# Optimization experiments

Measured on AMD Instinct MI355X. Metric: run time of the kernel, lower is better.

## Reference

```python
import jax, jax.numpy as jnp
import numpy as np

NEG_SLOPE = 0.2  # PyG GATConv default negative_slope
BN_EPS = 1e-5


def _segment_softmax(logits, seg, num_segments):
    # numerically stable softmax over edges grouped by destination node
    m = jax.ops.segment_max(logits, seg, num_segments=num_segments)
    e = jnp.exp(logits - m[seg])
    s = jax.ops.segment_sum(e, seg, num_segments=num_segments)
    return e / s[seg]


def _gat_conv(x, src, dst, W, a_src, a_dst, bias, heads, d_head, concat):
    N = x.shape[0]
    h = (x @ W).reshape(N, heads, d_head)                      # [N, H, D]
    alpha_src = jnp.einsum('nhd,hd->nh', h, a_src)             # [N, H]
    alpha_dst = jnp.einsum('nhd,hd->nh', h, a_dst)             # [N, H]
    logits = jax.nn.leaky_relu(alpha_src[src] + alpha_dst[dst], NEG_SLOPE)  # [E, H]
    alpha = _segment_softmax(logits, dst, N)                   # [E, H]
    msg = h[src] * alpha[:, :, None]                           # [E, H, D]
    out = jax.ops.segment_sum(msg, dst, num_segments=N)        # [N, H, D]
    out = out.reshape(N, heads * d_head) if concat else out.mean(axis=1)
    return out + bias


def setup_inputs() -> dict:
    key = jax.random.key(0)
    ks = jax.random.split(key, 12)
    N, E = 50000, 800000
    in_dim, hidden, out_dim, heads = 256, 128, 2, 4
    d1 = hidden // heads  # 32
    s = 0.05
    return {
        'x': jax.random.normal(ks[0], (N, in_dim), dtype=jnp.float32),
        'edge_index': jax.random.randint(ks[1], (2, E), 0, N, dtype=jnp.int64),
        'W1': jax.random.normal(ks[2], (in_dim, heads * d1), dtype=jnp.float32) * s,
        'att_src1': jax.random.normal(ks[3], (heads, d1), dtype=jnp.float32) * s,
        'att_dst1': jax.random.normal(ks[4], (heads, d1), dtype=jnp.float32) * s,
        'b1': jnp.zeros((heads * d1,), dtype=jnp.float32),
        'bn_gamma': jnp.ones((hidden,), dtype=jnp.float32),
        'bn_beta': jnp.zeros((hidden,), dtype=jnp.float32),
        'bn_mean': jnp.zeros((hidden,), dtype=jnp.float32),
        'bn_var': jnp.ones((hidden,), dtype=jnp.float32),
        'W2': jax.random.normal(ks[5], (hidden, out_dim), dtype=jnp.float32) * s,
        'att_src2': jax.random.normal(ks[6], (1, out_dim), dtype=jnp.float32) * s,
        'att_dst2': jax.random.normal(ks[7], (1, out_dim), dtype=jnp.float32) * s,
        'b2': jnp.zeros((out_dim,), dtype=jnp.float32),
    }


def reference(x, edge_index, W1, att_src1, att_dst1, b1,
              bn_gamma, bn_beta, bn_mean, bn_var,
              W2, att_src2, att_dst2, b2):
    N = x.shape[0]
    # PyG GATConv adds self-loops by default
    loop = jnp.arange(N, dtype=edge_index.dtype)
    src = jnp.concatenate([edge_index[0], loop])
    dst = jnp.concatenate([edge_index[1], loop])

    heads, d1 = att_src1.shape
    h = _gat_conv(x, src, dst, W1, att_src1, att_dst1, b1, heads, d1, concat=True)
    # BatchNorm1d in eval mode (running stats), then ReLU (dropout is a no-op in eval)
    h = (h - bn_mean) * jax.lax.rsqrt(bn_var + BN_EPS) * bn_gamma + bn_beta
    h = jax.nn.relu(h)
    out = _gat_conv(h, src, dst, W2, att_src2, att_dst2, b2, 1, att_src2.shape[1], concat=False)
    return out
```

## Files before the change

### kernel.cpp

```cpp
#include <hip/hip_runtime.h>
#include <hip/hip_bf16.h>

#define LRELU(x) ((x) > 0.f ? (x) : 0.2f * (x))
#define CAP 96
#define BINBITS 7
#define BINCAP 2600

typedef short bf16x8 __attribute__((ext_vector_type(8)));
typedef float f32x4 __attribute__((ext_vector_type(4)));

__device__ __forceinline__ float b2f(unsigned short u) {
  union { unsigned int i; float f; } v;
  v.i = ((unsigned int)u) << 16;
  return v.f;
}
__device__ __forceinline__ unsigned short f2b(float f) {
  unsigned int u = __float_as_uint(f);
  unsigned int r = (u + 0x7fffu + ((u >> 16) & 1u)) >> 16;
  return (unsigned short)r;
}

__global__ __launch_bounds__(256) void prep_w1t_kernel(
    const float* __restrict__ W, unsigned short* __restrict__ w1t) {
  int idx = blockIdx.x * 256 + threadIdx.x;
  int n = idx >> 8, k = idx & 255;
  w1t[idx] = f2b(W[k * 128 + n]);
}

__global__ __launch_bounds__(256) void gemm1_mfma_kernel(
    const float* __restrict__ x, const unsigned short* __restrict__ w1t,
    const float* __restrict__ atts, const float* __restrict__ attd,
    unsigned short* __restrict__ h1bf, float* __restrict__ asrc,
    float* __restrict__ adst, int N) {
  __shared__ unsigned short bsh[128 * 264];

  const int tid = threadIdx.x;
#pragma unroll
  for (int i = 0; i < 16; i++) {
    int idx = (i * 256 + tid) * 8;
    int row = idx >> 8;
    int k = idx & 255;
    *(uint4*)(bsh + row * 264 + k) = *(const uint4*)(w1t + row * 256 + k);
  }
  __syncthreads();

  const int m0 = blockIdx.x * 64 + (tid >> 6) * 16;
  if (m0 >= N) return;
  const int lane = tid & 63;
  const int row = lane & 15;
  const int quad = lane >> 4;

  f32x4 acc[8];
#pragma unroll
  for (int t = 0; t < 8; t++) acc[t] = (f32x4){0.f, 0.f, 0.f, 0.f};

  const float* ap = x + (size_t)(m0 + row) * 256 + quad * 8;
#pragma unroll
  for (int k0 = 0; k0 < 256; k0 += 32) {
    float4 av0 = *(const float4*)(ap + k0);
    float4 av1 = *(const float4*)(ap + k0 + 4);
    float af[8] = {av0.x, av0.y, av0.z, av0.w, av1.x, av1.y, av1.z, av1.w};
    bf16x8 ahi, alo;
#pragma unroll
    for (int j = 0; j < 8; j++) {
      unsigned short h = f2b(af[j]);
      ahi[j] = (short)h;
      alo[j] = (short)f2b(af[j] - b2f(h));
    }
#pragma unroll
    for (int t = 0; t < 8; t++) {
      bf16x8 b = *(const bf16x8*)(bsh + (t * 16 + row) * 264 + k0 + quad * 8);
      acc[t] = __builtin_amdgcn_mfma_f32_16x16x32_bf16(ahi, b, acc[t], 0, 0, 0);
      acc[t] = __builtin_amdgcn_mfma_f32_16x16x32_bf16(alo, b, acc[t], 0, 0, 0);
    }
  }
  unsigned short* op = h1bf + (size_t)(m0 + quad * 4) * 128 + row;
#pragma unroll
  for (int t = 0; t < 8; t++)
#pragma unroll
    for (int r = 0; r < 4; r++)
      op[(size_t)r * 128 + t * 16] = f2b(acc[t][r]);

  float asv[8], adv[8];
#pragma unroll
  for (int t = 0; t < 8; t++) {
    asv[t] = atts[t * 16 + row];
    adv[t] = attd[t * 16 + row];
  }
  float ps[4][4], pd[4][4];
#pragma unroll
  for (int h = 0; h < 4; h++)
#pragma unroll
    for (int r = 0; r < 4; r++) {
      ps[h][r] = acc[2 * h][r] * asv[2 * h] + acc[2 * h + 1][r] * asv[2 * h + 1];
      pd[h][r] = acc[2 * h][r] * adv[2 * h] + acc[2 * h + 1][r] * adv[2 * h + 1];
    }
#pragma unroll
  for (int o = 1; o < 16; o <<= 1) {
#pragma unroll
    for (int h = 0; h < 4; h++)
#pragma unroll
      for (int r = 0; r < 4; r++) {
        ps[h][r] += __shfl_xor(ps[h][r], o);
        pd[h][r] += __shfl_xor(pd[h][r], o);
      }
  }
  if (row == 0) {
#pragma unroll
    for (int r = 0; r < 4; r++) {
      int m = m0 + quad * 4 + r;
#pragma unroll
      for (int h = 0; h < 4; h++) {
        asrc[m * 4 + h] = ps[h][r];
        adst[m * 4 + h] = pd[h][r];
      }
    }
  }
}

__global__ __launch_bounds__(256) void bin_edges_kernel(
    const int* __restrict__ ei, int E, int* __restrict__ gcnt,
    unsigned int* __restrict__ binned, int nbins) {
  __shared__ int hist[512];
  __shared__ int base[512];
  const int tid = threadIdx.x;
  for (int i = tid; i < 512; i += 256) hist[i] = 0;
  __syncthreads();
  const int chunk = (E + gridDim.x - 1) / gridDim.x;
  const int e0 = blockIdx.x * chunk;
  const int e1 = min(e0 + chunk, E);
  for (int e = e0 + tid; e < e1; e += 256)
    atomicAdd(&hist[ei[(size_t)E + e] >> BINBITS], 1);
  __syncthreads();
  for (int i = tid; i < nbins; i += 256)
    if (hist[i] > 0) base[i] = atomicAdd(&gcnt[i], hist[i]);
  __syncthreads();
  for (int i = tid; i < 512; i += 256) hist[i] = 0;
  __syncthreads();
  for (int e = e0 + tid; e < e1; e += 256) {
    int s = ei[e];
    int t = ei[(size_t)E + e];
    int b = t >> BINBITS;
    int pos = base[b] + atomicAdd(&hist[b], 1);
    if (pos < BINCAP)
      binned[(size_t)b * BINCAP + pos] = ((unsigned int)t << 16) | (unsigned int)s;
  }
}

__global__ __launch_bounds__(256) void bin_to_buckets_kernel(
    const int* __restrict__ gcnt, const unsigned int* __restrict__ binned,
    int* __restrict__ cnt, unsigned short* __restrict__ buckets, int N) {
  __shared__ unsigned short lbkt[128 * CAP];
  __shared__ int lcnt[128];
  const int b = blockIdx.x;
  const int tid = threadIdx.x;
  if (tid < 128) lcnt[tid] = 0;
  __syncthreads();
  const int ne = min(gcnt[b], BINCAP);
  const unsigned int* bp = binned + (size_t)b * BINCAP;
  for (int i = tid; i < ne; i += 256) {
    unsigned int p = bp[i];
    int ln = (p >> 16) & 127;
    int pos = atomicAdd(&lcnt[ln], 1);
    if (pos < CAP) lbkt[ln * CAP + pos] = (unsigned short)(p & 0xffff);
  }
  __syncthreads();
  const int n0 = b << BINBITS;
  const int nn = min(128, N - n0);
  if (nn <= 0) return;
  if (tid < nn) cnt[n0 + tid] = lcnt[tid];
  const int total8 = (nn * CAP) >> 3;
  uint4* d4 = (uint4*)(buckets + (size_t)n0 * CAP);
  const uint4* s4 = (const uint4*)lbkt;
  for (int i = tid; i < total8; i += 256) d4[i] = s4[i];
}

__global__ __launch_bounds__(256) void agg1_kernel(
    const int* __restrict__ cnt, const unsigned short* __restrict__ buckets,
    const unsigned short* __restrict__ h1bf, const float* __restrict__ asrc,
    const float* __restrict__ adst, const float* __restrict__ b1,
    const float* __restrict__ gamma, const float* __restrict__ beta,
    const float* __restrict__ mean, const float* __restrict__ var,
    const float* __restrict__ W2, const float* __restrict__ as2,
    const float* __restrict__ ad2, float4* __restrict__ pk, int N) {
  const int wv = __builtin_amdgcn_readfirstlane(threadIdx.x >> 6);
  const int t = blockIdx.x * 4 + wv;
  if (t >= N) return;
  const int l = threadIdx.x & 63;
  const int h = l >> 4;
  const float ad = adst[t * 4 + h];

  float acc0 = 0.f, acc1 = 0.f, den = 0.f;
  const unsigned short* bkt = buckets + (size_t)t * CAP;
  const int deg = min(__builtin_amdgcn_readfirstlane(cnt[t]), CAP);
  int j = 0;
  for (; j + 4 <= deg; j += 4) {
    int s0 = __builtin_amdgcn_readfirstlane((int)bkt[j]);
    int s1 = __builtin_amdgcn_readfirstlane((int)bkt[j + 1]);
    int s2 = __builtin_amdgcn_readfirstlane((int)bkt[j + 2]);
    int s3 = __builtin_amdgcn_readfirstlane((int)bkt[j + 3]);
    unsigned int p0 = *(const unsigned int*)(h1bf + (size_t)s0 * 128 + 2 * l);
    unsigned int p1 = *(const unsigned int*)(h1bf + (size_t)s1 * 128 + 2 * l);
    unsigned int p2 = *(const unsigned int*)(h1bf + (size_t)s2 * 128 + 2 * l);
    unsigned int p3 = *(const unsigned int*)(h1bf + (size_t)s3 * 128 + 2 * l);
    float w0 = __expf(LRELU(asrc[s0 * 4 + h] + ad));
    float w1 = __expf(LRELU(asrc[s1 * 4 + h] + ad));
    float w2 = __expf(LRELU(asrc[s2 * 4 + h] + ad));
    float w3 = __expf(LRELU(asrc[s3 * 4 + h] + ad));
    acc0 += w0 * b2f((unsigned short)(p0 & 0xffff)) +
            w1 * b2f((unsigned short)(p1 & 0xffff)) +
            w2 * b2f((unsigned short)(p2 & 0xffff)) +
            w3 * b2f((unsigned short)(p3 & 0xffff));
    acc1 += w0 * b2f((unsigned short)(p0 >> 16)) +
            w1 * b2f((unsigned short)(p1 >> 16)) +
            w2 * b2f((unsigned short)(p2 >> 16)) +
            w3 * b2f((unsigned short)(p3 >> 16));
    den += w0 + w1 + w2 + w3;
  }
  for (; j < deg; j++) {
    int s0 = __builtin_amdgcn_readfirstlane((int)bkt[j]);
    unsigned int p0 = *(const unsigned int*)(h1bf + (size_t)s0 * 128 + 2 * l);
    float w0 = __expf(LRELU(asrc[s0 * 4 + h] + ad));
    acc0 += w0 * b2f((unsigned short)(p0 & 0xffff));
    acc1 += w0 * b2f((unsigned short)(p0 >> 16));
    den += w0;
  }
  {
    unsigned int p0 = *(const unsigned int*)(h1bf + (size_t)t * 128 + 2 * l);
    float w0 = __expf(LRELU(asrc[t * 4 + h] + ad));
    acc0 += w0 * b2f((unsigned short)(p0 & 0xffff));
    acc1 += w0 * b2f((unsigned short)(p0 >> 16));
    den += w0;
  }
  const int c0 = 2 * l;
  float inv = 1.f / den;
  float v0 = acc0 * inv + b1[c0];
  float v1 = acc1 * inv + b1[c0 + 1];
  v0 = (v0 - mean[c0]) * rsqrtf(var[c0] + 1e-5f) * gamma[c0] + beta[c0];
  v1 = (v1 - mean[c0 + 1]) * rsqrtf(var[c0 + 1] + 1e-5f) * gamma[c0 + 1] +
       beta[c0 + 1];
  v0 = v0 > 0.f ? v0 : 0.f;
  v1 = v1 > 0.f ? v1 : 0.f;

  float g0 = v0 * W2[c0 * 2 + 0] + v1 * W2[(c0 + 1) * 2 + 0];
  float g1 = v0 * W2[c0 * 2 + 1] + v1 * W2[(c0 + 1) * 2 + 1];
#pragma unroll
  for (int o = 32; o > 0; o >>= 1) {
    g0 += __shfl_down(g0, o);
    g1 += __shfl_down(g1, o);
  }
  if (l == 0) {
    float4 p;
    p.x = g0;
    p.y = g1;
    p.z = g0 * as2[0] + g1 * as2[1];
    p.w = g0 * ad2[0] + g1 * ad2[1];
    pk[t] = p;
  }
}

__global__ __launch_bounds__(256) void agg2_kernel(
    const int* __restrict__ cnt, const unsigned short* __restrict__ buckets,
    const float4* __restrict__ pk, const float* __restrict__ b2,
    float* __restrict__ out, int N) {
  const int t = blockIdx.x * 16 + (threadIdx.x >> 4);
  if (t >= N) return;
  const int lg = threadIdx.x & 15;
  float4 pt = pk[t];
  const float ad = pt.w;
  float a0 = 0.f, a1 = 0.f, den = 0.f;
  const unsigned short* bkt = buckets + (size_t)t * CAP;
  const int deg = min(cnt[t], CAP);
  for (int j = lg; j < deg; j += 16) {
    float4 p = pk[bkt[j]];
    float w = __expf(LRELU(p.z + ad));
    a0 += w * p.x;
    a1 += w * p.y;
    den += w;
  }
#pragma unroll
  for (int o = 8; o > 0; o >>= 1) {
    a0 += __shfl_xor(a0, o);
    a1 += __shfl_xor(a1, o);
    den += __shfl_xor(den, o);
  }
  if (lg == 0) {
    float w = __expf(LRELU(pt.z + ad));
    a0 += w * pt.x;
    a1 += w * pt.y;
    den += w;
    float2 o2;
    o2.x = a0 / den + b2[0];
    o2.y = a1 / den + b2[1];
    *(float2*)(out + (size_t)t * 2) = o2;
  }
}

extern "C" void kernel_launch(void* const* d_in, const int* in_sizes, int n_in,
                              void* d_out, int out_size, void* d_ws,
                              size_t ws_size, hipStream_t stream) {
  const float* x      = (const float*)d_in[0];
  const int*   ei     = (const int*)d_in[1];
  const float* W1     = (const float*)d_in[2];
  const float* atts1  = (const float*)d_in[3];
  const float* attd1  = (const float*)d_in[4];
  const float* b1     = (const float*)d_in[5];
  const float* gamma  = (const float*)d_in[6];
  const float* beta   = (const float*)d_in[7];
  const float* mean   = (const float*)d_in[8];
  const float* var    = (const float*)d_in[9];
  const float* W2     = (const float*)d_in[10];
  const float* atts2  = (const float*)d_in[11];
  const float* attd2  = (const float*)d_in[12];
  const float* b2     = (const float*)d_in[13];
  float* out = (float*)d_out;

  const int N = in_sizes[0] / 256;
  const int E = in_sizes[1] / 2;
  const int nbins = (N + (1 << BINBITS) - 1) >> BINBITS;

  char* ws = (char*)d_ws;
  size_t off = 0;
  unsigned short* h1bf = (unsigned short*)(ws + off); off += (size_t)N * 128 * 2;
  float* asrc1 = (float*)(ws + off); off += (size_t)N * 4 * 4;
  float* adst1 = (float*)(ws + off); off += (size_t)N * 4 * 4;
  float4* pk   = (float4*)(ws + off); off += (size_t)N * 16;
  int*   cnt   = (int*)  (ws + off); off += (size_t)N * 4;
  int*   gcnt  = (int*)  (ws + off); off += 512 * 4;
  unsigned short* w1t = (unsigned short*)(ws + off); off += 128 * 256 * 2;
  unsigned short* buckets = (unsigned short*)(ws + off);
  off += (size_t)N * CAP * 2;
  unsigned int* binned = (unsigned int*)(ws + off);
  off += (size_t)nbins * BINCAP * 4;

  hipMemsetAsync(gcnt, 0, 512 * 4, stream);
  bin_edges_kernel<<<512, 256, 0, stream>>>(ei, E, gcnt, binned, nbins);
  bin_to_buckets_kernel<<<nbins, 256, 0, stream>>>(gcnt, binned, cnt, buckets,
                                                   N);

  prep_w1t_kernel<<<128, 256, 0, stream>>>(W1, w1t);
  gemm1_mfma_kernel<<<(N + 63) / 64, 256, 0, stream>>>(
      x, w1t, atts1, attd1, h1bf, asrc1, adst1, N);
  agg1_kernel<<<(N + 3) / 4, 256, 0, stream>>>(cnt, buckets, h1bf, asrc1,
                                               adst1, b1, gamma, beta, mean,
                                               var, W2, atts2, attd2, pk, N);

  agg2_kernel<<<(N + 15) / 16, 256, 0, stream>>>(cnt, buckets, pk, b2, out, N);
}
```

Before: 209.0 us.

## Split wave into four edge groups with 16-byte row loads in agg1

The layer-1 aggregation now has each wavefront handle four neighbor edges at once. Each 16-lane group loads a full 256-byte bf16 row with uint4 loads, where before the whole wave walked one edge at a time with 4-byte loads per lane. Partial sums are combined across the groups with xor shuffles. After the final reduction the result is scaled by 0.25 because all four groups hold the identical post-BN values. This targets latency-bound per-edge gathers and scalar readfirstlane serialization, at the cost of eight accumulators per lane and lanes idling in the tail iteration.

```diff
diff --git a/kernel.cpp b/kernel.cpp
--- a/kernel.cpp
+++ b/kernel.cpp
@@ -187,75 +187,82 @@
   const int t = blockIdx.x * 4 + wv;
   if (t >= N) return;
   const int l = threadIdx.x & 63;
-  const int h = l >> 4;
-  const float ad = adst[t * 4 + h];
-
-  float acc0 = 0.f, acc1 = 0.f, den = 0.f;
+  const int g = l >> 4;
+  const int p = l & 15;
+  const int hd = p >> 2;
+  const float ad = adst[t * 4 + hd];
+
+  float acc[8];
+#pragma unroll
+  for (int k = 0; k < 8; k++) acc[k] = 0.f;
+  float den = 0.f;
+
   const unsigned short* bkt = buckets + (size_t)t * CAP;
   const int deg = min(__builtin_amdgcn_readfirstlane(cnt[t]), CAP);
-  int j = 0;
-  for (; j + 4 <= deg; j += 4) {
-    int s0 = __builtin_amdgcn_readfirstlane((int)bkt[j]);
-    int s1 = __builtin_amdgcn_readfirstlane((int)bkt[j + 1]);
-    int s2 = __builtin_amdgcn_readfirstlane((int)bkt[j + 2]);
-    int s3 = __builtin_amdgcn_readfirstlane((int)bkt[j + 3]);
-    unsigned int p0 = *(const unsigned int*)(h1bf + (size_t)s0 * 128 + 2 * l);
-    unsigned int p1 = *(const unsigned int*)(h1bf + (size_t)s1 * 128 + 2 * l);
-    unsigned int p2 = *(const unsigned int*)(h1bf + (size_t)s2 * 128 + 2 * l);
-    unsigned int p3 = *(const unsigned int*)(h1bf + (size_t)s3 * 128 + 2 * l);
-    float w0 = __expf(LRELU(asrc[s0 * 4 + h] + ad));
-    float w1 = __expf(LRELU(asrc[s1 * 4 + h] + ad));
-    float w2 = __expf(LRELU(asrc[s2 * 4 + h] + ad));
-    float w3 = __expf(LRELU(asrc[s3 * 4 + h] + ad));
-    acc0 += w0 * b2f((unsigned short)(p0 & 0xffff)) +
-            w1 * b2f((unsigned short)(p1 & 0xffff)) +
-            w2 * b2f((unsigned short)(p2 & 0xffff)) +
-            w3 * b2f((unsigned short)(p3 & 0xffff));
-    acc1 += w0 * b2f((unsigned short)(p0 >> 16)) +
-            w1 * b2f((unsigned short)(p1 >> 16)) +
-            w2 * b2f((unsigned short)(p2 >> 16)) +
-            w3 * b2f((unsigned short)(p3 >> 16));
-    den += w0 + w1 + w2 + w3;
-  }
-  for (; j < deg; j++) {
-    int s0 = __builtin_amdgcn_readfirstlane((int)bkt[j]);
-    unsigned int p0 = *(const unsigned int*)(h1bf + (size_t)s0 * 128 + 2 * l);
-    float w0 = __expf(LRELU(asrc[s0 * 4 + h] + ad));
-    acc0 += w0 * b2f((unsigned short)(p0 & 0xffff));
-    acc1 += w0 * b2f((unsigned short)(p0 >> 16));
-    den += w0;
-  }
-  {
-    unsigned int p0 = *(const unsigned int*)(h1bf + (size_t)t * 128 + 2 * l);
-    float w0 = __expf(LRELU(asrc[t * 4 + h] + ad));
-    acc0 += w0 * b2f((unsigned short)(p0 & 0xffff));
-    acc1 += w0 * b2f((unsigned short)(p0 >> 16));
-    den += w0;
-  }
-  const int c0 = 2 * l;
-  float inv = 1.f / den;
-  float v0 = acc0 * inv + b1[c0];
-  float v1 = acc1 * inv + b1[c0 + 1];
-  v0 = (v0 - mean[c0]) * rsqrtf(var[c0] + 1e-5f) * gamma[c0] + beta[c0];
-  v1 = (v1 - mean[c0 + 1]) * rsqrtf(var[c0 + 1] + 1e-5f) * gamma[c0 + 1] +
-       beta[c0 + 1];
-  v0 = v0 > 0.f ? v0 : 0.f;
-  v1 = v1 > 0.f ? v1 : 0.f;
-
-  float g0 = v0 * W2[c0 * 2 + 0] + v1 * W2[(c0 + 1) * 2 + 0];
-  float g1 = v0 * W2[c0 * 2 + 1] + v1 * W2[(c0 + 1) * 2 + 1];
+  const int total = deg + 1;
+
+  for (int j = 0; j < total; j += 4) {
+    const int i = j + g;
+    int s = t;
+    if (i < deg) s = bkt[i];
+    uint4 r = *(const uint4*)(h1bf + (size_t)s * 128 + p * 8);
+    float w = 0.f;
+    if (i < total) {
+      float lg = asrc[s * 4 + hd] + ad;
+      w = __expf(LRELU(lg));
+    }
+    acc[0] += w * b2f((unsigned short)(r.x & 0xffff));
+    acc[1] += w * b2f((unsigned short)(r.x >> 16));
+    acc[2] += w * b2f((unsigned short)(r.y & 0xffff));
+    acc[3] += w * b2f((unsigned short)(r.y >> 16));
+    acc[4] += w * b2f((unsigned short)(r.z & 0xffff));
+    acc[5] += w * b2f((unsigned short)(r.z >> 16));
+    acc[6] += w * b2f((unsigned short)(r.w & 0xffff));
+    acc[7] += w * b2f((unsigned short)(r.w >> 16));
+    den += w;
+  }
+#pragma unroll
+  for (int o = 16; o <= 32; o <<= 1) {
+#pragma unroll
+    for (int k = 0; k < 8; k++) acc[k] += __shfl_xor(acc[k], o);
+    den += __shfl_xor(den, o);
+  }
+
+  const int c0 = p * 8;
+  const float inv = 1.f / den;
+  float4 b1a = *(const float4*)(b1 + c0), b1b = *(const float4*)(b1 + c0 + 4);
+  float4 mna = *(const float4*)(mean + c0), mnb = *(const float4*)(mean + c0 + 4);
+  float4 vra = *(const float4*)(var + c0), vrb = *(const float4*)(var + c0 + 4);
+  float4 gma = *(const float4*)(gamma + c0), gmb = *(const float4*)(gamma + c0 + 4);
+  float4 bta = *(const float4*)(beta + c0), btb = *(const float4*)(beta + c0 + 4);
+  float bb[8] = {b1a.x, b1a.y, b1a.z, b1a.w, b1b.x, b1b.y, b1b.z, b1b.w};
+  float mn[8] = {mna.x, mna.y, mna.z, mna.w, mnb.x, mnb.y, mnb.z, mnb.w};
+  float vr[8] = {vra.x, vra.y, vra.z, vra.w, vrb.x, vrb.y, vrb.z, vrb.w};
+  float gm[8] = {gma.x, gma.y, gma.z, gma.w, gmb.x, gmb.y, gmb.z, gmb.w};
+  float bt[8] = {bta.x, bta.y, bta.z, bta.w, btb.x, btb.y, btb.z, btb.w};
+  float g0 = 0.f, g1 = 0.f;
+#pragma unroll
+  for (int k = 0; k < 8; k++) {
+    float v = acc[k] * inv + bb[k];
+    v = (v - mn[k]) * rsqrtf(vr[k] + 1e-5f) * gm[k] + bt[k];
+    v = v > 0.f ? v : 0.f;
+    g0 += v * W2[(c0 + k) * 2 + 0];
+    g1 += v * W2[(c0 + k) * 2 + 1];
+  }
 #pragma unroll
   for (int o = 32; o > 0; o >>= 1) {
     g0 += __shfl_down(g0, o);
     g1 += __shfl_down(g1, o);
   }
   if (l == 0) {
-    float4 p;
-    p.x = g0;
-    p.y = g1;
-    p.z = g0 * as2[0] + g1 * as2[1];
-    p.w = g0 * ad2[0] + g1 * ad2[1];
-    pk[t] = p;
+    g0 *= 0.25f;
+    g1 *= 0.25f;
+    float4 pv;
+    pv.x = g0;
+    pv.y = g1;
+    pv.z = g0 * as2[0] + g1 * as2[1];
+    pv.w = g0 * ad2[0] + g1 * ad2[1];
+    pk[t] = pv;
   }
 }
 
```

New measurement: 211.3 us. Within noise of the previous version (+1.1%).

## Replace fine-grained edge binning with coarse superbins and block-staged coalesced writes

Applied to the files above, without the earlier changes.

Edge binning now scatters edges into 7 coarse superbins of 8192 destination nodes, staging each 256-edge tile in shared memory so the global writes are grouped per superbin. Before, edges were scattered into ~391 small bins with nearly random global writes. Each bucket-building block now scans its whole superbin (~115K entries) and keeps only the entries belonging to its 128-node bin. That multiplies the read traffic in the second pass by about 64x, though the reads are coalesced and largely shared through L2.

```diff
diff --git a/kernel.cpp b/kernel.cpp
--- a/kernel.cpp
+++ b/kernel.cpp
@@ -4,7 +4,9 @@
 #define LRELU(x) ((x) > 0.f ? (x) : 0.2f * (x))
 #define CAP 96
 #define BINBITS 7
-#define BINCAP 2600
+#define SBBITS 13
+#define NSB 7
+#define SBCAP 136000
 
 typedef short bf16x8 __attribute__((ext_vector_type(8)));
 typedef float f32x4 __attribute__((ext_vector_type(4)));
@@ -118,37 +120,59 @@
   }
 }
 
-__global__ __launch_bounds__(256) void bin_edges_kernel(
-    const int* __restrict__ ei, int E, int* __restrict__ gcnt,
-    unsigned int* __restrict__ binned, int nbins) {
-  __shared__ int hist[512];
-  __shared__ int base[512];
+__global__ __launch_bounds__(256) void superbin_kernel(
+    const int* __restrict__ ei, int E, int* __restrict__ gsb,
+    unsigned int* __restrict__ sbin) {
+  __shared__ int hist[NSB], base[NSB], binstart[NSB], cur[NSB];
+  __shared__ unsigned int stage[256];
+  __shared__ int gposs[256];
   const int tid = threadIdx.x;
-  for (int i = tid; i < 512; i += 256) hist[i] = 0;
-  __syncthreads();
-  const int chunk = (E + gridDim.x - 1) / gridDim.x;
-  const int e0 = blockIdx.x * chunk;
-  const int e1 = min(e0 + chunk, E);
-  for (int e = e0 + tid; e < e1; e += 256)
-    atomicAdd(&hist[ei[(size_t)E + e] >> BINBITS], 1);
-  __syncthreads();
-  for (int i = tid; i < nbins; i += 256)
-    if (hist[i] > 0) base[i] = atomicAdd(&gcnt[i], hist[i]);
-  __syncthreads();
-  for (int i = tid; i < 512; i += 256) hist[i] = 0;
-  __syncthreads();
-  for (int e = e0 + tid; e < e1; e += 256) {
-    int s = ei[e];
-    int t = ei[(size_t)E + e];
-    int b = t >> BINBITS;
-    int pos = base[b] + atomicAdd(&hist[b], 1);
-    if (pos < BINCAP)
-      binned[(size_t)b * BINCAP + pos] = ((unsigned int)t << 16) | (unsigned int)s;
-  }
-}
-
-__global__ __launch_bounds__(256) void bin_to_buckets_kernel(
-    const int* __restrict__ gcnt, const unsigned int* __restrict__ binned,
+
+  for (int e0 = blockIdx.x * 256; e0 < E; e0 += gridDim.x * 256) {
+    const int e = e0 + tid;
+    const bool valid = e < E;
+    int s = 0, t = 0, sb = 0;
+    if (valid) {
+      s = ei[e];
+      t = ei[(size_t)E + e];
+      sb = t >> SBBITS;
+    }
+    if (tid < NSB) hist[tid] = 0;
+    __syncthreads();
+    if (valid) atomicAdd(&hist[sb], 1);
+    __syncthreads();
+    if (tid < NSB) {
+      int c = hist[tid];
+      base[tid] = c ? atomicAdd(&gsb[tid], c) : 0;
+    }
+    if (tid == 0) {
+      int acc2 = 0;
+      for (int i = 0; i < NSB; i++) {
+        binstart[i] = acc2;
+        cur[i] = acc2;
+        acc2 += hist[i];
+      }
+    }
+    __syncthreads();
+    if (valid) {
+      int loc = atomicAdd(&cur[sb], 1);
+      stage[loc] = ((unsigned int)t << 16) | (unsigned int)s;
+      int r = loc - binstart[sb];
+      int gp = base[sb] + r;
+      gposs[loc] = (gp < SBCAP) ? (sb * SBCAP + gp) : -1;
+    }
+    __syncthreads();
+    const int ne = min(256, E - e0);
+    if (tid < ne) {
+      int gp = gposs[tid];
+      if (gp >= 0) sbin[gp] = stage[tid];
+    }
+    __syncthreads();
+  }
+}
+
+__global__ __launch_bounds__(256) void sbin_to_buckets_kernel(
+    const int* __restrict__ gsb, const unsigned int* __restrict__ sbin,
     int* __restrict__ cnt, unsigned short* __restrict__ buckets, int N) {
   __shared__ unsigned short lbkt[128 * CAP];
   __shared__ int lcnt[128];
@@ -156,13 +180,17 @@
   const int tid = threadIdx.x;
   if (tid < 128) lcnt[tid] = 0;
   __syncthreads();
-  const int ne = min(gcnt[b], BINCAP);
-  const unsigned int* bp = binned + (size_t)b * BINCAP;
+  const int sb = b >> (SBBITS - BINBITS);
+  const int ne = min(gsb[sb], SBCAP);
+  const unsigned int* bp = sbin + (size_t)sb * SBCAP;
+  const unsigned int want = (unsigned int)b;
   for (int i = tid; i < ne; i += 256) {
     unsigned int p = bp[i];
-    int ln = (p >> 16) & 127;
-    int pos = atomicAdd(&lcnt[ln], 1);
-    if (pos < CAP) lbkt[ln * CAP + pos] = (unsigned short)(p & 0xffff);
+    if ((p >> (16 + BINBITS)) == want) {
+      int ln = (p >> 16) & 127;
+      int pos = atomicAdd(&lcnt[ln], 1);
+      if (pos < CAP) lbkt[ln * CAP + pos] = (unsigned short)(p & 0xffff);
+    }
   }
   __syncthreads();
   const int n0 = b << BINBITS;
@@ -326,17 +354,16 @@
   float* adst1 = (float*)(ws + off); off += (size_t)N * 4 * 4;
   float4* pk   = (float4*)(ws + off); off += (size_t)N * 16;
   int*   cnt   = (int*)  (ws + off); off += (size_t)N * 4;
-  int*   gcnt  = (int*)  (ws + off); off += 512 * 4;
+  int*   gsb   = (int*)  (ws + off); off += 64 * 4;
   unsigned short* w1t = (unsigned short*)(ws + off); off += 128 * 256 * 2;
   unsigned short* buckets = (unsigned short*)(ws + off);
   off += (size_t)N * CAP * 2;
-  unsigned int* binned = (unsigned int*)(ws + off);
-  off += (size_t)nbins * BINCAP * 4;
-
-  hipMemsetAsync(gcnt, 0, 512 * 4, stream);
-  bin_edges_kernel<<<512, 256, 0, stream>>>(ei, E, gcnt, binned, nbins);
-  bin_to_buckets_kernel<<<nbins, 256, 0, stream>>>(gcnt, binned, cnt, buckets,
-                                                   N);
+  unsigned int* sbin = (unsigned int*)(ws + off);
+  off += (size_t)NSB * SBCAP * 4;
+
+  hipMemsetAsync(gsb, 0, 64 * 4, stream);
+  superbin_kernel<<<512, 256, 0, stream>>>(ei, E, gsb, sbin);
+  sbin_to_buckets_kernel<<<nbins, 256, 0, stream>>>(gsb, sbin, cnt, buckets, N);
 
   prep_w1t_kernel<<<128, 256, 0, stream>>>(W1, w1t);
   gemm1_mfma_kernel<<<(N + 63) / 64, 256, 0, stream>>>(
```

Result: slower. 369.2 us (+76.7%).
